# Kernel optimization log

Measured on AMD Instinct MI355X. Metric: run time of the kernel, lower is better.

The kernel has to match this reference:

```python
import jax, jax.numpy as jnp
import numpy as np

N = 100_000   # number of sparse points
C = 128       # channels
K3 = 27       # 3x3x3 kernel offsets


def sparse_conv(x, nbr, W, b):
    """Minkowski-style sparse conv: gather-GEMM-scatter.
    x:   [N, Cin] point features
    nbr: [N, K3] neighbor index per kernel offset; index N -> missing (zero row)
    W:   [K3, Cin, Cout], b: [Cout]
    """
    x_pad = jnp.concatenate([x, jnp.zeros((1, x.shape[1]), x.dtype)], axis=0)

    def step(acc, wk_nk):
        Wk, nk = wk_nk                      # Wk: [Cin,Cout], nk: [N]
        return acc + x_pad[nk] @ Wk, None   # gather + GEMM, accumulate

    acc0 = jnp.broadcast_to(b, (x.shape[0], W.shape[2])).astype(x.dtype)
    acc, _ = jax.lax.scan(step, acc0, (W, nbr.T))
    return acc


def setup_inputs() -> dict:
    key = jax.random.key(0)
    ks = jax.random.split(key, 12)
    Ch = C // 2

    def w(k, shape, fan_in):
        return jax.random.normal(k, shape, dtype=jnp.float32) / np.sqrt(fan_in)

    x = jax.random.normal(ks[0], (N, C), dtype=jnp.float32)
    # neighbor map; value N means "no neighbor" (maps to zero-padded row)
    nbr = jax.random.randint(ks[1], (N, K3), 0, N + 1, dtype=jnp.int32)

    return {
        "x": x,
        "nbr": nbr,
        "W00": w(ks[2], (K3, C, Ch), K3 * C),   # conv0_0: kxkxk, C -> C/2
        "b00": jnp.zeros((Ch,), jnp.float32),
        "W01": w(ks[3], (K3, Ch, Ch), K3 * Ch),  # conv0_1: kxkxk, C/2 -> C/2
        "b01": jnp.zeros((Ch,), jnp.float32),
        "W10": w(ks[4], (C, Ch), C),             # conv1_0: 1x1x1, C -> C/2
        "b10": jnp.zeros((Ch,), jnp.float32),
        "W11": w(ks[5], (K3, Ch, Ch), K3 * Ch),  # conv1_1: kxkxk, C/2 -> C/2
        "b11": jnp.zeros((Ch,), jnp.float32),
        "W12": w(ks[6], (Ch, Ch), Ch),           # conv1_2: 1x1x1, C/2 -> C/2
        "b12": jnp.zeros((Ch,), jnp.float32),
    }


def reference(x, nbr, W00, b00, W01, b01, W10, b10, W11, b11, W12, b12):
    # branch 0: conv -> relu -> conv
    h0 = jax.nn.relu(sparse_conv(x, nbr, W00, b00))
    out0 = sparse_conv(h0, nbr, W01, b01)
    # branch 1: 1x1 conv -> relu -> conv -> relu -> 1x1 conv
    h1 = jax.nn.relu(x @ W10 + b10)
    h1 = jax.nn.relu(sparse_conv(h1, nbr, W11, b11))
    out1 = h1 @ W12 + b12
    # concat channels, residual add
    return jnp.concatenate([out0, out1], axis=1) + x
```

## Files before the change

### kernel.cpp

```cpp
#include <hip/hip_runtime.h>
#include <hip/hip_bf16.h>
#include <stdint.h>

typedef __bf16 bf16x8 __attribute__((ext_vector_type(8)));
typedef float  f32x4  __attribute__((ext_vector_type(4)));

#define MFMA(A, B, C) __builtin_amdgcn_mfma_f32_16x16x32_bf16((A), (B), (C), 0, 0, 0)

static __device__ __forceinline__ unsigned short f2b(float f) {
    union { float f; unsigned int u; } v; v.f = f;
    return (unsigned short)((v.u + 0x7FFFu + ((v.u >> 16) & 1u)) >> 16);
}

__global__ __launch_bounds__(256) void convert_kernel(
    const float* __restrict__ x, unsigned short* __restrict__ xb,
    unsigned short* __restrict__ hb, int N) {
    long long i = (long long)blockIdx.x * blockDim.x + threadIdx.x;
    long long base = i * 4;
    long long nx = (long long)N * 128;
    long long total = nx + 128;
    if (base >= total) return;
    if (base < nx) {
        float4 v = *(const float4*)(x + base);
        ushort4 o;
        o.x = f2b(v.x); o.y = f2b(v.y); o.z = f2b(v.z); o.w = f2b(v.w);
        *(ushort4*)(xb + base) = o;
    } else {
        ushort4 z = make_ushort4(0, 0, 0, 0);
        *(ushort4*)(xb + base) = z;
        *(ushort4*)(hb + base) = z;
    }
}

__global__ __launch_bounds__(256) void pack_kernel(
    const float* __restrict__ W00, const float* __restrict__ W01,
    const float* __restrict__ W10, const float* __restrict__ W11,
    const float* __restrict__ W12,
    unsigned short* __restrict__ wp00, unsigned short* __restrict__ wpC,
    unsigned short* __restrict__ wp10, unsigned short* __restrict__ wp12) {
    int g = blockIdx.x * blockDim.x + threadIdx.x;
    const float* W; int cinSteps; int which;
    if (g < 27648)      { W = W00; cinSteps = 4; which = 0; }
    else if (g < 41472) { g -= 27648; W = W01; cinSteps = 2; which = 1; }
    else if (g < 55296) { g -= 41472; W = W11; cinSteps = 2; which = 2; }
    else if (g < 56320) { g -= 55296; W = W10; cinSteps = 4; which = 3; }
    else if (g < 56832) { g -= 56320; W = W12; cinSteps = 2; which = 4; }
    else return;
    int lane = g & 63;
    int st   = g >> 6;
    int t    = st & 3;
    int s    = st >> 2;
    int q = lane >> 4, n16 = lane & 15;
    int k    = s / cinSteps;
    int cinb = (s % cinSteps) * 32;
    int Cin  = cinSteps * 32;
    int cout = t * 16 + n16;
    unsigned short o[8];
#pragma unroll
    for (int j = 0; j < 8; ++j) {
        float v = W[(size_t)(k * Cin + cinb + q * 8 + j) * 64 + cout];
        o[j] = f2b(v);
    }
    unsigned short* dst;
    if (which == 0)      dst = wp00 + (size_t)g * 8;
    else if (which == 1) dst = wpC + (size_t)k * 8192 +
                               ((size_t)(((s & 1) * 4 + t) * 64 + lane)) * 8;
    else if (which == 2) dst = wpC + (size_t)k * 8192 + 4096 +
                               ((size_t)(((s & 1) * 4 + t) * 64 + lane)) * 8;
    else if (which == 3) dst = wp10 + (size_t)g * 8;
    else                 dst = wp12 + (size_t)g * 8;
    *(ushort4*)(dst)     = make_ushort4(o[0], o[1], o[2], o[3]);
    *(ushort4*)(dst + 4) = make_ushort4(o[4], o[5], o[6], o[7]);
}

__global__ __launch_bounds__(256, 2) void passB_kernel(
    const unsigned short* __restrict__ xb, const int* __restrict__ nbr,
    const unsigned short* __restrict__ wp00, const unsigned short* __restrict__ wp10,
    const float* __restrict__ b00, const float* __restrict__ b10,
    unsigned short* __restrict__ hb, int N) {
    __shared__ __align__(16) unsigned short bbuf[2][8192];
    int tid = threadIdx.x;
    int lane = tid & 63;
    int wv   = tid >> 6;
    int q = lane >> 4, n16 = lane & 15;
    int rowbase = blockIdx.x * 128 + wv * 32;

    f32x4 acc0[2][4];
    f32x4 acc1[2][4];
#pragma unroll
    for (int rs = 0; rs < 2; ++rs)
#pragma unroll
        for (int t = 0; t < 4; ++t) { acc0[rs][t] = (f32x4)0.f; acc1[rs][t] = (f32x4)0.f; }

    int mc0 = min(rowbase + n16, N - 1);
    int mc1 = min(rowbase + 16 + n16, N - 1);
    size_t nb0 = (size_t)mc0 * 27, nb1 = (size_t)mc1 * 27;

    int ia = nbr[nb0], ib = nbr[nb1];
    int4 br[4];
#pragma unroll
    for (int j = 0; j < 4; ++j) br[j] = *(const int4*)(wp00 + j * 2048 + tid * 8);
    bf16x8 A0c[4], A1c[4];
    {
        const unsigned short* p0 = xb + (size_t)ia * 128 + q * 8;
        const unsigned short* p1 = xb + (size_t)ib * 128 + q * 8;
#pragma unroll
        for (int s2 = 0; s2 < 4; ++s2) {
            A0c[s2] = *(const bf16x8*)(p0 + s2 * 32);
            A1c[s2] = *(const bf16x8*)(p1 + s2 * 32);
        }
    }
    int ian = nbr[nb0 + 1], ibn = nbr[nb1 + 1];
#pragma unroll
    for (int j = 0; j < 4; ++j) *(int4*)(&bbuf[0][j * 2048 + tid * 8]) = br[j];
    __syncthreads();

    for (int k = 0; k < 27; ++k) {
        int buf = k & 1;
        if (k < 26) {
            const unsigned short* src = wp00 + (size_t)(k + 1) * 8192;
#pragma unroll
            for (int j = 0; j < 4; ++j) br[j] = *(const int4*)(src + j * 2048 + tid * 8);
        }
        int ia2 = (k + 2 < 27) ? nbr[nb0 + k + 2] : mc0;
        int ib2 = (k + 2 < 27) ? nbr[nb1 + k + 2] : mc1;
        bf16x8 A0n[4], A1n[4];
        {
            const unsigned short* p0 = xb + (size_t)ian * 128 + q * 8;
            const unsigned short* p1 = xb + (size_t)ibn * 128 + q * 8;
#pragma unroll
            for (int s2 = 0; s2 < 4; ++s2) {
                A0n[s2] = *(const bf16x8*)(p0 + s2 * 32);
                A1n[s2] = *(const bf16x8*)(p1 + s2 * 32);
            }
        }
        const unsigned short* lb = &bbuf[buf][0];
#pragma unroll
        for (int s2 = 0; s2 < 4; ++s2)
#pragma unroll
            for (int t = 0; t < 4; ++t) {
                bf16x8 B = *(const bf16x8*)(lb + (s2 * 4 + t) * 512 + lane * 8);
                acc0[0][t] = MFMA(A0c[s2], B, acc0[0][t]);
                acc0[1][t] = MFMA(A1c[s2], B, acc0[1][t]);
            }
        if (k < 26) {
#pragma unroll
            for (int j = 0; j < 4; ++j)
                *(int4*)(&bbuf[buf ^ 1][j * 2048 + tid * 8]) = br[j];
        }
#pragma unroll
        for (int s2 = 0; s2 < 4; ++s2) { A0c[s2] = A0n[s2]; A1c[s2] = A1n[s2]; }
        ian = ia2; ibn = ib2;
        __syncthreads();
    }

#pragma unroll
    for (int s2 = 0; s2 < 4; ++s2)
#pragma unroll
        for (int t = 0; t < 4; ++t) {
            bf16x8 B = *(const bf16x8*)(wp10 + s2 * 2048 + t * 512 + lane * 8);
            acc1[0][t] = MFMA(A0c[s2], B, acc1[0][t]);
            acc1[1][t] = MFMA(A1c[s2], B, acc1[1][t]);
        }

#pragma unroll
    for (int rs = 0; rs < 2; ++rs)
#pragma unroll
        for (int t = 0; t < 4; ++t) {
            int col = t * 16 + n16;
            float bb0 = b00[col], bb1 = b10[col];
#pragma unroll
            for (int r = 0; r < 4; ++r) {
                int row = rowbase + rs * 16 + q * 4 + r;
                if (row < N) {
                    hb[(size_t)row * 128 + col]      = f2b(fmaxf(acc0[rs][t][r] + bb0, 0.f));
                    hb[(size_t)row * 128 + 64 + col] = f2b(fmaxf(acc1[rs][t][r] + bb1, 0.f));
                }
            }
        }
}

__global__ __launch_bounds__(256, 2) void passC_kernel(
    const unsigned short* __restrict__ hb, const int* __restrict__ nbr,
    const float* __restrict__ x,
    const unsigned short* __restrict__ wpC, const unsigned short* __restrict__ wp12,
    const float* __restrict__ b01, const float* __restrict__ b11,
    const float* __restrict__ b12, float* __restrict__ out, int N) {
    __shared__ __align__(16) unsigned short bbuf[2][8192];
    int tid = threadIdx.x;
    int lane = tid & 63;
    int wv   = tid >> 6;
    int q = lane >> 4, n16 = lane & 15;
    int rowbase = blockIdx.x * 128 + wv * 32;

    f32x4 accO0[2][4];
    f32x4 accT[2][4];
#pragma unroll
    for (int rs = 0; rs < 2; ++rs)
#pragma unroll
        for (int t = 0; t < 4; ++t) { accO0[rs][t] = (f32x4)0.f; accT[rs][t] = (f32x4)0.f; }

    int mc0 = min(rowbase + n16, N - 1);
    int mc1 = min(rowbase + 16 + n16, N - 1);
    size_t nb0 = (size_t)mc0 * 27, nb1 = (size_t)mc1 * 27;

    int ia = nbr[nb0], ib = nbr[nb1];
    int4 br[4];
#pragma unroll
    for (int j = 0; j < 4; ++j) br[j] = *(const int4*)(wpC + j * 2048 + tid * 8);
    bf16x8 A0c[2], C0c[2], A1c[2], C1c[2];
    {
        const unsigned short* p0 = hb + (size_t)ia * 128 + q * 8;
        const unsigned short* p1 = hb + (size_t)ib * 128 + q * 8;
#pragma unroll
        for (int s2 = 0; s2 < 2; ++s2) {
            A0c[s2] = *(const bf16x8*)(p0 + s2 * 32);
            C0c[s2] = *(const bf16x8*)(p0 + 64 + s2 * 32);
            A1c[s2] = *(const bf16x8*)(p1 + s2 * 32);
            C1c[s2] = *(const bf16x8*)(p1 + 64 + s2 * 32);
        }
    }
    int ian = nbr[nb0 + 1], ibn = nbr[nb1 + 1];
#pragma unroll
    for (int j = 0; j < 4; ++j) *(int4*)(&bbuf[0][j * 2048 + tid * 8]) = br[j];
    __syncthreads();

    for (int k = 0; k < 27; ++k) {
        int buf = k & 1;
        if (k < 26) {
            const unsigned short* src = wpC + (size_t)(k + 1) * 8192;
#pragma unroll
            for (int j = 0; j < 4; ++j) br[j] = *(const int4*)(src + j * 2048 + tid * 8);
        }
        int ia2 = (k + 2 < 27) ? nbr[nb0 + k + 2] : N;
        int ib2 = (k + 2 < 27) ? nbr[nb1 + k + 2] : N;
        bf16x8 A0n[2], C0n[2], A1n[2], C1n[2];
        {
            const unsigned short* p0 = hb + (size_t)ian * 128 + q * 8;
            const unsigned short* p1 = hb + (size_t)ibn * 128 + q * 8;
#pragma unroll
            for (int s2 = 0; s2 < 2; ++s2) {
                A0n[s2] = *(const bf16x8*)(p0 + s2 * 32);
                C0n[s2] = *(const bf16x8*)(p0 + 64 + s2 * 32);
                A1n[s2] = *(const bf16x8*)(p1 + s2 * 32);
                C1n[s2] = *(const bf16x8*)(p1 + 64 + s2 * 32);
            }
        }
        const unsigned short* lb = &bbuf[buf][0];
#pragma unroll
        for (int s2 = 0; s2 < 2; ++s2) {
#pragma unroll
            for (int t = 0; t < 4; ++t) {
                bf16x8 B = *(const bf16x8*)(lb + (s2 * 4 + t) * 512 + lane * 8);
                accO0[0][t] = MFMA(A0c[s2], B, accO0[0][t]);
                accO0[1][t] = MFMA(A1c[s2], B, accO0[1][t]);
            }
#pragma unroll
            for (int t = 0; t < 4; ++t) {
                bf16x8 B2 = *(const bf16x8*)(lb + 4096 + (s2 * 4 + t) * 512 + lane * 8);
                accT[0][t] = MFMA(C0c[s2], B2, accT[0][t]);
                accT[1][t] = MFMA(C1c[s2], B2, accT[1][t]);
            }
        }
        if (k < 26) {
#pragma unroll
            for (int j = 0; j < 4; ++j)
                *(int4*)(&bbuf[buf ^ 1][j * 2048 + tid * 8]) = br[j];
        }
#pragma unroll
        for (int s2 = 0; s2 < 2; ++s2) {
            A0c[s2] = A0n[s2]; C0c[s2] = C0n[s2];
            A1c[s2] = A1n[s2]; C1c[s2] = C1n[s2];
        }
        ian = ia2; ibn = ib2;
        __syncthreads();
    }

    unsigned short* scratch = &bbuf[0][0];
    unsigned short* myl = scratch + wv * 2304;
#pragma unroll
    for (int rs = 0; rs < 2; ++rs)
#pragma unroll
        for (int t = 0; t < 4; ++t) {
            int col = t * 16 + n16;
            float bo = b01[col], bt = b11[col];
#pragma unroll
            for (int r = 0; r < 4; ++r) {
                int row = rowbase + rs * 16 + q * 4 + r;
                if (row < N) {
                    float xv = __builtin_nontemporal_load(x + (size_t)row * 128 + col);
                    __builtin_nontemporal_store(accO0[rs][t][r] + bo + xv,
                                                out + (size_t)row * 128 + col);
                }
                float tv = fmaxf(accT[rs][t][r] + bt, 0.f);
                myl[(rs * 16 + q * 4 + r) * 72 + col] = f2b(tv);
            }
        }

    f32x4 accO1[2][4];
#pragma unroll
    for (int rs = 0; rs < 2; ++rs)
#pragma unroll
        for (int t = 0; t < 4; ++t) accO1[rs][t] = (f32x4)0.f;
#pragma unroll
    for (int s2 = 0; s2 < 2; ++s2) {
        bf16x8 A0 = *(const bf16x8*)(myl + n16 * 72 + s2 * 32 + q * 8);
        bf16x8 A1 = *(const bf16x8*)(myl + (16 + n16) * 72 + s2 * 32 + q * 8);
#pragma unroll
        for (int t = 0; t < 4; ++t) {
            bf16x8 B = *(const bf16x8*)(wp12 + s2 * 2048 + t * 512 + lane * 8);
            accO1[0][t] = MFMA(A0, B, accO1[0][t]);
            accO1[1][t] = MFMA(A1, B, accO1[1][t]);
        }
    }
#pragma unroll
    for (int rs = 0; rs < 2; ++rs)
#pragma unroll
        for (int t = 0; t < 4; ++t) {
            int col = t * 16 + n16;
            float bo = b12[col];
#pragma unroll
            for (int r = 0; r < 4; ++r) {
                int row = rowbase + rs * 16 + q * 4 + r;
                if (row < N) {
                    float xv = __builtin_nontemporal_load(x + (size_t)row * 128 + 64 + col);
                    __builtin_nontemporal_store(accO1[rs][t][r] + bo + xv,
                                                out + (size_t)row * 128 + 64 + col);
                }
            }
        }
}

extern "C" void kernel_launch(void* const* d_in, const int* in_sizes, int n_in,
                              void* d_out, int out_size, void* d_ws, size_t ws_size,
                              hipStream_t stream) {
    const float* x   = (const float*)d_in[0];
    const int*   nbr = (const int*)d_in[1];
    const float* W00 = (const float*)d_in[2];
    const float* b00 = (const float*)d_in[3];
    const float* W01 = (const float*)d_in[4];
    const float* b01 = (const float*)d_in[5];
    const float* W10 = (const float*)d_in[6];
    const float* b10 = (const float*)d_in[7];
    const float* W11 = (const float*)d_in[8];
    const float* b11 = (const float*)d_in[9];
    const float* W12 = (const float*)d_in[10];
    const float* b12 = (const float*)d_in[11];
    float* out = (float*)d_out;
    int N = in_sizes[0] / 128;

    char* ws = (char*)d_ws;
    size_t cur = 0;
    unsigned short* xb  = (unsigned short*)(ws + cur); cur += (size_t)(N + 1) * 128 * 2;
    unsigned short* hb  = (unsigned short*)(ws + cur); cur += (size_t)(N + 1) * 128 * 2;
    unsigned short* wp00 = (unsigned short*)(ws + cur); cur += 27648 * 8 * 2;
    unsigned short* wpC  = (unsigned short*)(ws + cur); cur += (size_t)27 * 8192 * 2;
    unsigned short* wp10 = (unsigned short*)(ws + cur); cur += 8192 * 2;
    unsigned short* wp12 = (unsigned short*)(ws + cur); cur += 4096 * 2;

    long long cvt_groups = ((long long)N * 128 + 128) / 4;
    int cvt_blocks = (int)((cvt_groups + 255) / 256);
    convert_kernel<<<cvt_blocks, 256, 0, stream>>>(x, xb, hb, N);
    pack_kernel<<<222, 256, 0, stream>>>(W00, W01, W10, W11, W12,
                                         wp00, wpC, wp10, wp12);
    int blocks = (N + 127) / 128;
    passB_kernel<<<blocks, 256, 0, stream>>>(xb, nbr, wp00, wp10, b00, b10, hb, N);
    passC_kernel<<<blocks, 256, 0, stream>>>(hb, nbr, x, wpC, wp12,
                                             b01, b11, b12, out, N);
}
```

Baseline: 437.8 us.

## Stage neighbor indices in LDS and gather rows contiguously with bpermute shuffle

Each block now loads its 128x27 slice of the neighbor table into LDS once, replacing per-iteration global index loads with LDS reads. Gathered rows are now fetched so that four adjacent lanes read contiguous 16-byte chunks of the same row, which coalesces better than the previous per-lane pattern. The data is then rearranged into MFMA fragment layout with ds_bpermute. This adds LDS usage (about 13.5 KB per block, which may hurt occupancy) and extra permute instructions in the inner loop. Index prefetch depth also drops from two steps ahead to one.

```diff
diff --git a/kernel.cpp b/kernel.cpp
--- a/kernel.cpp
+++ b/kernel.cpp
@@ -10,6 +10,14 @@
 static __device__ __forceinline__ unsigned short f2b(float f) {
     union { float f; unsigned int u; } v; v.f = f;
     return (unsigned short)((v.u + 0x7FFFu + ((v.u >> 16) & 1u)) >> 16);
+}
+
+static __device__ __forceinline__ bf16x8 perm_frag(int sel, bf16x8 D) {
+    union { bf16x8 v; int d[4]; } u, r;
+    u.v = D;
+#pragma unroll
+    for (int w = 0; w < 4; ++w) r.d[w] = __builtin_amdgcn_ds_bpermute(sel, u.d[w]);
+    return r.v;
 }
 
 __global__ __launch_bounds__(256) void convert_kernel(
@@ -79,11 +87,29 @@
     const float* __restrict__ b00, const float* __restrict__ b10,
     unsigned short* __restrict__ hb, int N) {
     __shared__ __align__(16) unsigned short bbuf[2][8192];
+    __shared__ int lds_idx[128 * 27];
     int tid = threadIdx.x;
     int lane = tid & 63;
     int wv   = tid >> 6;
     int q = lane >> 4, n16 = lane & 15;
+    int rowq = lane >> 2, chunk = lane & 3;
+    int sel = (n16 * 4 + q) * 4;
     int rowbase = blockIdx.x * 128 + wv * 32;
+
+    {
+        long long gbase = (long long)blockIdx.x * 128 * 27;
+        long long lim = (long long)N * 27 - 1;
+        for (int i = tid; i < 3456; i += 256) {
+            long long gi = gbase + i; if (gi > lim) gi = lim;
+            lds_idx[i] = nbr[gi];
+        }
+    }
+    int4 br[4];
+#pragma unroll
+    for (int j = 0; j < 4; ++j) br[j] = *(const int4*)(wp00 + j * 2048 + tid * 8);
+#pragma unroll
+    for (int j = 0; j < 4; ++j) *(int4*)(&bbuf[0][j * 2048 + tid * 8]) = br[j];
+    __syncthreads();
 
     f32x4 acc0[2][4];
     f32x4 acc1[2][4];
@@ -92,28 +118,22 @@
 #pragma unroll
         for (int t = 0; t < 4; ++t) { acc0[rs][t] = (f32x4)0.f; acc1[rs][t] = (f32x4)0.f; }
 
-    int mc0 = min(rowbase + n16, N - 1);
-    int mc1 = min(rowbase + 16 + n16, N - 1);
-    size_t nb0 = (size_t)mc0 * 27, nb1 = (size_t)mc1 * 27;
-
-    int ia = nbr[nb0], ib = nbr[nb1];
-    int4 br[4];
-#pragma unroll
-    for (int j = 0; j < 4; ++j) br[j] = *(const int4*)(wp00 + j * 2048 + tid * 8);
-    bf16x8 A0c[4], A1c[4];
+    int idxb0 = (wv * 32 + rowq) * 27;
+    int idxb1 = (wv * 32 + 16 + rowq) * 27;
+    int own0 = min(rowbase + rowq, N - 1);
+    int own1 = min(rowbase + 16 + rowq, N - 1);
+
+    int ia = lds_idx[idxb0], ib = lds_idx[idxb1];
+    bf16x8 D0[4], D1[4];
     {
-        const unsigned short* p0 = xb + (size_t)ia * 128 + q * 8;
-        const unsigned short* p1 = xb + (size_t)ib * 128 + q * 8;
+        const unsigned short* p0 = xb + (size_t)ia * 128 + chunk * 8;
+        const unsigned short* p1 = xb + (size_t)ib * 128 + chunk * 8;
 #pragma unroll
         for (int s2 = 0; s2 < 4; ++s2) {
-            A0c[s2] = *(const bf16x8*)(p0 + s2 * 32);
-            A1c[s2] = *(const bf16x8*)(p1 + s2 * 32);
-        }
-    }
-    int ian = nbr[nb0 + 1], ibn = nbr[nb1 + 1];
-#pragma unroll
-    for (int j = 0; j < 4; ++j) *(int4*)(&bbuf[0][j * 2048 + tid * 8]) = br[j];
-    __syncthreads();
+            D0[s2] = *(const bf16x8*)(p0 + s2 * 32);
+            D1[s2] = *(const bf16x8*)(p1 + s2 * 32);
+        }
+    }
 
     for (int k = 0; k < 27; ++k) {
         int buf = k & 1;
@@ -122,46 +142,51 @@
 #pragma unroll
             for (int j = 0; j < 4; ++j) br[j] = *(const int4*)(src + j * 2048 + tid * 8);
         }
-        int ia2 = (k + 2 < 27) ? nbr[nb0 + k + 2] : mc0;
-        int ib2 = (k + 2 < 27) ? nbr[nb1 + k + 2] : mc1;
-        bf16x8 A0n[4], A1n[4];
+        int ian = (k + 1 < 27) ? lds_idx[idxb0 + k + 1] : own0;
+        int ibn = (k + 1 < 27) ? lds_idx[idxb1 + k + 1] : own1;
+        bf16x8 D0n[4], D1n[4];
         {
-            const unsigned short* p0 = xb + (size_t)ian * 128 + q * 8;
-            const unsigned short* p1 = xb + (size_t)ibn * 128 + q * 8;
+            const unsigned short* p0 = xb + (size_t)ian * 128 + chunk * 8;
+            const unsigned short* p1 = xb + (size_t)ibn * 128 + chunk * 8;
 #pragma unroll
             for (int s2 = 0; s2 < 4; ++s2) {
-                A0n[s2] = *(const bf16x8*)(p0 + s2 * 32);
-                A1n[s2] = *(const bf16x8*)(p1 + s2 * 32);
+                D0n[s2] = *(const bf16x8*)(p0 + s2 * 32);
+                D1n[s2] = *(const bf16x8*)(p1 + s2 * 32);
             }
         }
         const unsigned short* lb = &bbuf[buf][0];
 #pragma unroll
-        for (int s2 = 0; s2 < 4; ++s2)
+        for (int s2 = 0; s2 < 4; ++s2) {
+            bf16x8 A0 = perm_frag(sel, D0[s2]);
+            bf16x8 A1 = perm_frag(sel, D1[s2]);
 #pragma unroll
             for (int t = 0; t < 4; ++t) {
                 bf16x8 B = *(const bf16x8*)(lb + (s2 * 4 + t) * 512 + lane * 8);
-                acc0[0][t] = MFMA(A0c[s2], B, acc0[0][t]);
-                acc0[1][t] = MFMA(A1c[s2], B, acc0[1][t]);
-            }
+                acc0[0][t] = MFMA(A0, B, acc0[0][t]);
+                acc0[1][t] = MFMA(A1, B, acc0[1][t]);
+            }
+        }
         if (k < 26) {
 #pragma unroll
             for (int j = 0; j < 4; ++j)
                 *(int4*)(&bbuf[buf ^ 1][j * 2048 + tid * 8]) = br[j];
         }
 #pragma unroll
-        for (int s2 = 0; s2 < 4; ++s2) { A0c[s2] = A0n[s2]; A1c[s2] = A1n[s2]; }
-        ian = ia2; ibn = ib2;
+        for (int s2 = 0; s2 < 4; ++s2) { D0[s2] = D0n[s2]; D1[s2] = D1n[s2]; }
         __syncthreads();
     }
 
 #pragma unroll
-    for (int s2 = 0; s2 < 4; ++s2)
+    for (int s2 = 0; s2 < 4; ++s2) {
+        bf16x8 A0 = perm_frag(sel, D0[s2]);
+        bf16x8 A1 = perm_frag(sel, D1[s2]);
 #pragma unroll
         for (int t = 0; t < 4; ++t) {
             bf16x8 B = *(const bf16x8*)(wp10 + s2 * 2048 + t * 512 + lane * 8);
-            acc1[0][t] = MFMA(A0c[s2], B, acc1[0][t]);
-            acc1[1][t] = MFMA(A1c[s2], B, acc1[1][t]);
-        }
+            acc1[0][t] = MFMA(A0, B, acc1[0][t]);
+            acc1[1][t] = MFMA(A1, B, acc1[1][t]);
+        }
+    }
 
 #pragma unroll
     for (int rs = 0; rs < 2; ++rs)
@@ -187,11 +212,29 @@
     const float* __restrict__ b01, const float* __restrict__ b11,
     const float* __restrict__ b12, float* __restrict__ out, int N) {
     __shared__ __align__(16) unsigned short bbuf[2][8192];
+    __shared__ int lds_idx[128 * 27];
     int tid = threadIdx.x;
     int lane = tid & 63;
     int wv   = tid >> 6;
     int q = lane >> 4, n16 = lane & 15;
+    int rowq = lane >> 2, chunk = lane & 3;
+    int sel = (n16 * 4 + q) * 4;
     int rowbase = blockIdx.x * 128 + wv * 32;
+
+    {
+        long long gbase = (long long)blockIdx.x * 128 * 27;
+        long long lim = (long long)N * 27 - 1;
+        for (int i = tid; i < 3456; i += 256) {
+            long long gi = gbase + i; if (gi > lim) gi = lim;
+            lds_idx[i] = nbr[gi];
+        }
+    }
+    int4 br[4];
+#pragma unroll
+    for (int j = 0; j < 4; ++j) br[j] = *(const int4*)(wpC + j * 2048 + tid * 8);
+#pragma unroll
+    for (int j = 0; j < 4; ++j) *(int4*)(&bbuf[0][j * 2048 + tid * 8]) = br[j];
+    __syncthreads();
 
     f32x4 accO0[2][4];
     f32x4 accT[2][4];
@@ -200,30 +243,22 @@
 #pragma unroll
         for (int t = 0; t < 4; ++t) { accO0[rs][t] = (f32x4)0.f; accT[rs][t] = (f32x4)0.f; }
 
-    int mc0 = min(rowbase + n16, N - 1);
-    int mc1 = min(rowbase + 16 + n16, N - 1);
-    size_t nb0 = (size_t)mc0 * 27, nb1 = (size_t)mc1 * 27;
-
-    int ia = nbr[nb0], ib = nbr[nb1];
-    int4 br[4];
-#pragma unroll
-    for (int j = 0; j < 4; ++j) br[j] = *(const int4*)(wpC + j * 2048 + tid * 8);
-    bf16x8 A0c[2], C0c[2], A1c[2], C1c[2];
+    int idxb0 = (wv * 32 + rowq) * 27;
+    int idxb1 = (wv * 32 + 16 + rowq) * 27;
+
+    int ia = lds_idx[idxb0], ib = lds_idx[idxb1];
+    bf16x8 DA0[2], DC0[2], DA1[2], DC1[2];
     {
-        const unsigned short* p0 = hb + (size_t)ia * 128 + q * 8;
-        const unsigned short* p1 = hb + (size_t)ib * 128 + q * 8;
+        const unsigned short* p0 = hb + (size_t)ia * 128 + chunk * 8;
+        const unsigned short* p1 = hb + (size_t)ib * 128 + chunk * 8;
 #pragma unroll
         for (int s2 = 0; s2 < 2; ++s2) {
-            A0c[s2] = *(const bf16x8*)(p0 + s2 * 32);
-            C0c[s2] = *(const bf16x8*)(p0 + 64 + s2 * 32);
-            A1c[s2] = *(const bf16x8*)(p1 + s2 * 32);
-            C1c[s2] = *(const bf16x8*)(p1 + 64 + s2 * 32);
-        }
-    }
-    int ian = nbr[nb0 + 1], ibn = nbr[nb1 + 1];
-#pragma unroll
-    for (int j = 0; j < 4; ++j) *(int4*)(&bbuf[0][j * 2048 + tid * 8]) = br[j];
-    __syncthreads();
+            DA0[s2] = *(const bf16x8*)(p0 + s2 * 32);
+            DC0[s2] = *(const bf16x8*)(p0 + 64 + s2 * 32);
+            DA1[s2] = *(const bf16x8*)(p1 + s2 * 32);
+            DC1[s2] = *(const bf16x8*)(p1 + 64 + s2 * 32);
+        }
+    }
 
     for (int k = 0; k < 27; ++k) {
         int buf = k & 1;
@@ -232,47 +267,50 @@
 #pragma unroll
             for (int j = 0; j < 4; ++j) br[j] = *(const int4*)(src + j * 2048 + tid * 8);
         }
-        int ia2 = (k + 2 < 27) ? nbr[nb0 + k + 2] : N;
-        int ib2 = (k + 2 < 27) ? nbr[nb1 + k + 2] : N;
-        bf16x8 A0n[2], C0n[2], A1n[2], C1n[2];
-        {
-            const unsigned short* p0 = hb + (size_t)ian * 128 + q * 8;
-            const unsigned short* p1 = hb + (size_t)ibn * 128 + q * 8;
+        bf16x8 DA0n[2], DC0n[2], DA1n[2], DC1n[2];
+        if (k < 26) {
+            int ian = lds_idx[idxb0 + k + 1];
+            int ibn = lds_idx[idxb1 + k + 1];
+            const unsigned short* p0 = hb + (size_t)ian * 128 + chunk * 8;
+            const unsigned short* p1 = hb + (size_t)ibn * 128 + chunk * 8;
 #pragma unroll
             for (int s2 = 0; s2 < 2; ++s2) {
-                A0n[s2] = *(const bf16x8*)(p0 + s2 * 32);
-                C0n[s2] = *(const bf16x8*)(p0 + 64 + s2 * 32);
-                A1n[s2] = *(const bf16x8*)(p1 + s2 * 32);
-                C1n[s2] = *(const bf16x8*)(p1 + 64 + s2 * 32);
+                DA0n[s2] = *(const bf16x8*)(p0 + s2 * 32);
+                DC0n[s2] = *(const bf16x8*)(p0 + 64 + s2 * 32);
+                DA1n[s2] = *(const bf16x8*)(p1 + s2 * 32);
+                DC1n[s2] = *(const bf16x8*)(p1 + 64 + s2 * 32);
             }
         }
         const unsigned short* lb = &bbuf[buf][0];
 #pragma unroll
         for (int s2 = 0; s2 < 2; ++s2) {
+            bf16x8 A0 = perm_frag(sel, DA0[s2]);
+            bf16x8 A1 = perm_frag(sel, DA1[s2]);
 #pragma unroll
             for (int t = 0; t < 4; ++t) {
                 bf16x8 B = *(const bf16x8*)(lb + (s2 * 4 + t) * 512 + lane * 8);
-                accO0[0][t] = MFMA(A0c[s2], B, accO0[0][t]);
-                accO0[1][t] = MFMA(A1c[s2], B, accO0[1][t]);
-            }
+                accO0[0][t] = MFMA(A0, B, accO0[0][t]);
+                accO0[1][t] = MFMA(A1, B, accO0[1][t]);
+            }
+            bf16x8 C0 = perm_frag(sel, DC0[s2]);
+            bf16x8 C1 = perm_frag(sel, DC1[s2]);
 #pragma unroll
             for (int t = 0; t < 4; ++t) {
                 bf16x8 B2 = *(const bf16x8*)(lb + 4096 + (s2 * 4 + t) * 512 + lane * 8);
-                accT[0][t] = MFMA(C0c[s2], B2, accT[0][t]);
-                accT[1][t] = MFMA(C1c[s2], B2, accT[1][t]);
+                accT[0][t] = MFMA(C0, B2, accT[0][t]);
+                accT[1][t] = MFMA(C1, B2, accT[1][t]);
             }
         }
         if (k < 26) {
 #pragma unroll
             for (int j = 0; j < 4; ++j)
                 *(int4*)(&bbuf[buf ^ 1][j * 2048 + tid * 8]) = br[j];
-        }
-#pragma unroll
-        for (int s2 = 0; s2 < 2; ++s2) {
-            A0c[s2] = A0n[s2]; C0c[s2] = C0n[s2];
-            A1c[s2] = A1n[s2]; C1c[s2] = C1n[s2];
-        }
-        ian = ia2; ibn = ib2;
+#pragma unroll
+            for (int s2 = 0; s2 < 2; ++s2) {
+                DA0[s2] = DA0n[s2]; DC0[s2] = DC0n[s2];
+                DA1[s2] = DA1n[s2]; DC1[s2] = DC1n[s2];
+            }
+        }
         __syncthreads();
     }
 
```

Result: faster. 414.3 us (-5.4%).
